# Kernel tuning notes

Measured on AMD Instinct MI355X. Metric: run time of the kernel, lower is better.

The kernel has to match this reference:

```python
import jax, jax.numpy as jnp
import numpy as np

B = 256      # number of graphs
IN = 128     # input_dim
FD = 256     # feature_dim (dims[1])
HID = 256    # hidden_dim of attention block (dims[2])
OUT = 128    # final output dim (dims[3])
TXT = 512    # text_emb_dim

LENGTHS = np.asarray(128 + (np.arange(B) % 256), dtype=np.int64)  # ragged lens 128..383
N = int(LENGTHS.sum())  # 65408 total nodes
LMAX = int(LENGTHS.max())  # 383


def setup_inputs() -> dict:
    key = jax.random.key(0)
    ks = jax.random.split(key, 16)
    s = 0.02
    return {
        "input": jax.random.normal(ks[0], (N, IN), jnp.float32),
        "text_emb": jax.random.normal(ks[1], (B, TXT), jnp.float32),
        "repeat_list": jnp.asarray(LENGTHS),
        # layer 0: Linear(IN -> FD)
        "W0": jax.random.normal(ks[2], (IN, FD), jnp.float32) * s,
        "b0": jax.random.normal(ks[3], (FD,), jnp.float32) * s,
        # cross-attention block params
        "Wq": jax.random.normal(ks[4], (TXT, FD), jnp.float32) * s,
        "bq": jax.random.normal(ks[5], (FD,), jnp.float32) * s,
        "Wk": jax.random.normal(ks[6], (FD, FD), jnp.float32) * s,
        "bk": jax.random.normal(ks[7], (FD,), jnp.float32) * s,
        "Wv": jax.random.normal(ks[8], (FD, FD), jnp.float32) * s,
        "bv": jax.random.normal(ks[9], (FD,), jnp.float32) * s,
        "Wo": jax.random.normal(ks[10], (FD, HID), jnp.float32) * s,
        "bo": jax.random.normal(ks[11], (HID,), jnp.float32) * s,
        # layer 2: Linear(HID -> OUT), last layer (no activation)
        "W2": jax.random.normal(ks[12], (HID, OUT), jnp.float32) * s,
        "b2": jax.random.normal(ks[13], (OUT,), jnp.float32) * s,
    }


def _cross_attention(h, text_emb, repeat_list, Wq, bq, Wk, bk, Wv, bv, Wo, bo):
    # h: [N, FD] packed ragged node features; repeat_list: [B] lengths (constant ints)
    n = h.shape[0]
    b = repeat_list.shape[0]
    fd = h.shape[1]
    # pad ragged -> [B, LMAX, FD] (pad value 0) + validity mask
    seg = jnp.repeat(jnp.arange(b), repeat_list, total_repeat_length=n)  # [N] graph id
    offsets = jnp.cumsum(repeat_list) - repeat_list                      # [B] start of each graph
    pos = jnp.arange(n) - offsets[seg]                                   # [N] within-graph pos
    padded = jnp.zeros((b, LMAX, fd), h.dtype).at[seg, pos].set(h)
    valid = jnp.arange(LMAX)[None, :] < repeat_list[:, None]             # [B, L]

    q = text_emb @ Wq + bq                              # [B, FD]
    k = (padded @ Wk + bk) * valid[..., None]           # masked_fill(mask==0, 0)
    v = (padded @ Wv + bv) * valid[..., None]

    # query is broadcast identically over the padded-length axis, so each row of the
    # [L, L] score matrix is the same vector: scores[b, j] = q[b] . k[b, j]
    scores = jnp.einsum('bf,bjf->bj', q, k)             # [B, L]
    scores = jnp.where(valid, scores, -jnp.inf)         # mask invalid columns j
    p = jax.nn.softmax(scores, axis=-1)                 # [B, L]
    # output = attention^T @ value with identical rows => out[b,j,:] = p[b,j] * sum_i v[b,i,:]
    v_sum = v.sum(axis=1)                               # [B, FD] (padded rows already zero)
    out_pad = p[..., None] * v_sum[:, None, :]          # [B, L, FD]
    out_nodes = out_pad[seg, pos]                       # unpad-concat -> [N, FD]
    return out_nodes @ Wo + bo                          # [N, HID]


def reference(input, text_emb, repeat_list, W0, b0, Wq, bq, Wk, bk, Wv, bv, Wo, bo, W2, b2):
    h = jax.nn.relu(input @ W0 + b0)                                     # layer 0 + relu
    h = _cross_attention(h, text_emb, repeat_list, Wq, bq, Wk, bk, Wv, bv, Wo, bo)
    h = jax.nn.relu(h)                                                   # layer 1 + relu
    return h @ W2 + b2                                                   # layer 2 (last, no act)
```

## Files before the change

kernel.cpp:

```cpp
#include <hip/hip_runtime.h>
#include <math.h>

#define B_G   256
#define IN_D  128
#define FD    256
#define HID   256
#define OUT_D 128
#define TXT   512
#define XKS   136

typedef short bf16x8 __attribute__((ext_vector_type(8)));
typedef float f32x4  __attribute__((ext_vector_type(4)));

__device__ __forceinline__ unsigned bf_rne(float x) {
    unsigned u = __float_as_uint(x);
    u += 0x7fffu + ((u >> 16) & 1u);
    return u >> 16;
}
__device__ __forceinline__ float bf_to_f(unsigned h) {
    return __uint_as_float(h << 16);
}
__device__ __forceinline__ void split2(float a0, float a1, unsigned& hp, unsigned& lp) {
    unsigned h0 = bf_rne(a0), h1 = bf_rne(a1);
    float r0 = a0 - bf_to_f(h0), r1 = a1 - bf_to_f(h1);
    hp = h0 | (h1 << 16);
    lp = bf_rne(r0) | (bf_rne(r1) << 16);
}

__global__ __launch_bounds__(256) void k_prepA(
    const float* __restrict__ text_emb, const float* __restrict__ Wq,
    const float* __restrict__ bq, const float* __restrict__ Wk,
    const float* __restrict__ W0, const int* __restrict__ lens,
    float* __restrict__ qk, int* __restrict__ offsets, float* __restrict__ hsum,
    unsigned short* __restrict__ W0sH, unsigned short* __restrict__ W0sL)
{
    int blk = blockIdx.x, t = threadIdx.x;
    __shared__ float te[TXT];
    __shared__ float q[FD];
    __shared__ int   sc[B_G];

    if (blk < 256) {
        int b = blk;
        hsum[b * FD + t] = 0.f;
        for (int i = t; i < TXT; i += 256) te[i] = text_emb[(size_t)b * TXT + i];
        __syncthreads();
        float acc = bq[t];
        for (int k = 0; k < TXT; k++) acc = fmaf(te[k], Wq[k * FD + t], acc);
        q[t] = acc;
        __syncthreads();
        float a2 = 0.f;
        for (int f = 0; f < FD; f++) a2 = fmaf(Wk[t * FD + f], q[f], a2);
        qk[b * FD + t] = a2;
    } else if (blk < 260) {
        int e = (blk - 256) * 256 + t;
        int kc = e >> 8, c = e & 255;
        size_t base = (size_t)(kc * 256 + c) * 32;
        for (int kk = 0; kk < 32; kk++) {
            float v = W0[(size_t)(kc * 32 + kk) * FD + c];
            unsigned h = bf_rne(v);
            float r = v - bf_to_f(h);
            W0sH[base + kk] = (unsigned short)h;
            W0sL[base + kk] = (unsigned short)bf_rne(r);
        }
    } else {
        sc[t] = lens[t];
        __syncthreads();
        for (int d = 1; d < 256; d <<= 1) {
            int v = (t >= d) ? sc[t - d] : 0;
            __syncthreads();
            sc[t] += v;
            __syncthreads();
        }
        offsets[t + 1] = sc[t];
        if (t == 0) offsets[0] = 0;
    }
}

__global__ __launch_bounds__(256, 2) void k_l0_mfma(
    const float* __restrict__ X,
    const unsigned short* __restrict__ W0sH, const unsigned short* __restrict__ W0sL,
    const float* __restrict__ b0, const float* __restrict__ qk,
    const int* __restrict__ offsets,
    float* __restrict__ scores, float* __restrict__ hsum)
{
    int b = blockIdx.y;
    int off = offsets[b], len = offsets[b + 1] - off;
    int n0 = blockIdx.x * 64;
    if (n0 >= len) return;
    int nvalid = min(64, len - n0);

    __shared__ __align__(16) unsigned short XsH[64 * XKS], XsL[64 * XKS];
    __shared__ float qks[FD];
    __shared__ float bsh[FD];
    __shared__ float red[4][64];

    int tid = threadIdx.x;
    int lane = tid & 63, w = tid >> 6;
    int ln = lane & 15, quad = lane >> 4;

    qks[tid] = qk[b * FD + tid];
    bsh[tid] = b0[tid];

    {
        int node_s = tid >> 2, ks = (tid & 3) * 32;
        const float* Xr = X + (size_t)(off + n0 + node_s) * IN_D + ks;
        float xv[32];
        if (node_s < nvalid) {
#pragma unroll
            for (int q2 = 0; q2 < 8; q2++) {
                float4 v = ((const float4*)Xr)[q2];
                xv[q2 * 4 + 0] = v.x; xv[q2 * 4 + 1] = v.y;
                xv[q2 * 4 + 2] = v.z; xv[q2 * 4 + 3] = v.w;
            }
        } else {
#pragma unroll
            for (int q2 = 0; q2 < 32; q2++) xv[q2] = 0.f;
        }
#pragma unroll
        for (int g = 0; g < 4; g++) {
            uint4 hq, lq;
            split2(xv[g * 8 + 0], xv[g * 8 + 1], hq.x, lq.x);
            split2(xv[g * 8 + 2], xv[g * 8 + 3], hq.y, lq.y);
            split2(xv[g * 8 + 4], xv[g * 8 + 5], hq.z, lq.z);
            split2(xv[g * 8 + 6], xv[g * 8 + 7], hq.w, lq.w);
            *(uint4*)&XsH[node_s * XKS + ks + g * 8] = hq;
            *(uint4*)&XsL[node_s * XKS + ks + g * 8] = lq;
        }
    }
    __syncthreads();

    f32x4 acc[4][4] = {};
#pragma unroll
    for (int kc = 0; kc < 4; kc++) {
        bf16x8 AH[4], AL[4], BH[4], BL[4];
#pragma unroll
        for (int i = 0; i < 4; i++) {
            AH[i] = *(const bf16x8*)&XsH[(16 * i + ln) * XKS + kc * 32 + quad * 8];
            AL[i] = *(const bf16x8*)&XsL[(16 * i + ln) * XKS + kc * 32 + quad * 8];
        }
#pragma unroll
        for (int j = 0; j < 4; j++) {
            int c = 64 * w + 16 * j + ln;
            size_t base = (size_t)(kc * 256 + c) * 32 + quad * 8;
            BH[j] = *(const bf16x8*)&W0sH[base];
            BL[j] = *(const bf16x8*)&W0sL[base];
        }
#pragma unroll
        for (int i = 0; i < 4; i++)
#pragma unroll
            for (int j = 0; j < 4; j++) {
                acc[i][j] = __builtin_amdgcn_mfma_f32_16x16x32_bf16(AH[i], BH[j], acc[i][j], 0, 0, 0);
                acc[i][j] = __builtin_amdgcn_mfma_f32_16x16x32_bf16(AH[i], BL[j], acc[i][j], 0, 0, 0);
                acc[i][j] = __builtin_amdgcn_mfma_f32_16x16x32_bf16(AL[i], BH[j], acc[i][j], 0, 0, 0);
            }
    }

    float sp[4][4];
    float cs[4] = {0.f, 0.f, 0.f, 0.f};
#pragma unroll
    for (int i = 0; i < 4; i++)
#pragma unroll
        for (int r = 0; r < 4; r++) sp[i][r] = 0.f;

#pragma unroll
    for (int i = 0; i < 4; i++)
#pragma unroll
        for (int j = 0; j < 4; j++) {
            int c = 64 * w + 16 * j + ln;
            float bb = bsh[c], qv = qks[c];
#pragma unroll
            for (int r = 0; r < 4; r++) {
                int node = 16 * i + 4 * quad + r;
                float h = acc[i][j][r] + bb;
                h = (h > 0.f && node < nvalid) ? h : 0.f;
                sp[i][r] = fmaf(h, qv, sp[i][r]);
                cs[j] += h;
            }
        }
#pragma unroll
    for (int i = 0; i < 4; i++)
#pragma unroll
        for (int r = 0; r < 4; r++) {
            float s = sp[i][r];
            s += __shfl_xor(s, 1); s += __shfl_xor(s, 2);
            s += __shfl_xor(s, 4); s += __shfl_xor(s, 8);
            sp[i][r] = s;
        }
    if (ln == 0) {
#pragma unroll
        for (int i = 0; i < 4; i++)
#pragma unroll
            for (int r = 0; r < 4; r++)
                red[w][16 * i + 4 * quad + r] = sp[i][r];
    }
#pragma unroll
    for (int j = 0; j < 4; j++) {
        float s = cs[j];
        s += __shfl_xor(s, 16); s += __shfl_xor(s, 32);
        if (quad == 0) atomicAdd(&hsum[b * FD + 64 * w + 16 * j + ln], s);
    }
    __syncthreads();
    if (tid < 64 && tid < nvalid)
        scores[off + n0 + tid] = red[0][tid] + red[1][tid] + red[2][tid] + red[3][tid];
}

__global__ __launch_bounds__(1024) void k_graph(
    const float* __restrict__ scores, const float* __restrict__ hsum,
    const float* __restrict__ Wv, const float* __restrict__ bv,
    const float* __restrict__ Wo, const int* __restrict__ offsets,
    float* __restrict__ wvec, float* __restrict__ smax, float* __restrict__ dinv)
{
    int b = blockIdx.x, tid = threadIdx.x;
    int t = tid & 255, g = tid >> 8;
    int off = offsets[b], len = offsets[b + 1] - off;
    __shared__ float redm[16], reds[16];
    __shared__ float hs[FD], vs[FD];
    __shared__ float part[4][FD];

    float m = -INFINITY;
    for (int i = tid; i < len; i += 1024) m = fmaxf(m, scores[off + i]);
    for (int d = 1; d < 64; d <<= 1) m = fmaxf(m, __shfl_xor(m, d));
    if ((tid & 63) == 0) redm[tid >> 6] = m;
    __syncthreads();
    m = -INFINITY;
#pragma unroll
    for (int k = 0; k < 16; k++) m = fmaxf(m, redm[k]);

    float s = 0.f;
    for (int i = tid; i < len; i += 1024) s += expf(scores[off + i] - m);
    for (int d = 1; d < 64; d <<= 1) s += __shfl_xor(s, d);
    if ((tid & 63) == 0) reds[tid >> 6] = s;
    if (g == 0) hs[t] = hsum[b * FD + t];
    __syncthreads();
    s = 0.f;
#pragma unroll
    for (int k = 0; k < 16; k++) s += reds[k];

    float acc = (g == 0) ? (float)len * bv[t] : 0.f;
    for (int f = 64 * g; f < 64 * g + 64; f++) acc = fmaf(hs[f], Wv[f * FD + t], acc);
    part[g][t] = acc;
    __syncthreads();
    if (g == 0) vs[t] = part[0][t] + part[1][t] + part[2][t] + part[3][t];
    __syncthreads();
    float a2 = 0.f;
    for (int f = 64 * g; f < 64 * g + 64; f++) a2 = fmaf(vs[f], Wo[f * HID + t], a2);
    part[g][t] = a2;
    __syncthreads();
    if (g == 0) wvec[b * HID + t] = part[0][t] + part[1][t] + part[2][t] + part[3][t];
    if (tid == 0) { smax[b] = m; dinv[b] = 1.0f / s; }
}

__global__ __launch_bounds__(1024) void k_fin_walk(
    const float* __restrict__ scores, const float* __restrict__ wvec,
    const float* __restrict__ bo, const float* __restrict__ W2,
    const float* __restrict__ b2, const float* __restrict__ smax,
    const float* __restrict__ dinv, const int* __restrict__ offsets,
    float* __restrict__ Y)
{
    int b = blockIdx.x, tid = threadIdx.x;
    int off = offsets[b], len = offsets[b + 1] - off;

    __shared__ float tOrig[256];
    __shared__ float tS[256], dwS[256], dbS[256];
    __shared__ int   kS[256];
    __shared__ float wS[256], boS[256];
    __shared__ int   cnt[257], startS[257];
    __shared__ float A0s[OUT_D], C0s[OUT_D], b2s[OUT_D];
    __shared__ float segA[8][OUT_D], segC[8][OUT_D];
    __shared__ __align__(16) char ops_raw[656 * 16];
    float* opA = (float*)ops_raw;
    float* opB = (float*)(ops_raw + 2624);
    int*   opN = (int*)(ops_raw + 5248);
    int*   opK = (int*)(ops_raw + 7872);

    float m = smax[b], di = dinv[b];

    bool real = false;
    if (tid < 256) {
        float wv = wvec[b * HID + tid];
        float bv = bo[tid];
        wS[tid] = wv; boS[tid] = bv;
        bool isev = (wv > 0.f && bv < 0.f) || (wv < 0.f && bv > 0.f);
        float tk = isev ? (-bv / wv) : INFINITY;
        real = isev && (tk < INFINITY);
        tOrig[tid] = real ? tk : INFINITY;
        cnt[tid] = 0;
        if (tid == 0) cnt[256] = 0;
    }
    if (tid < OUT_D) b2s[tid] = b2[tid];
    __syncthreads();

    if (tid < 256) {
        float tk = tOrig[tid];
        int r = 0;
        for (int j = 0; j < 256; j++) {
            float tj = tOrig[j];
            r += (tj < tk || (tj == tk && j < tid)) ? 1 : 0;
        }
        tS[r] = tk;
        kS[r] = tid;
        float wv = wS[tid], bv = boS[tid];
        dwS[r] = real ? fabsf(wv) : 0.f;
        dbS[r] = real ? -fabsf(bv) : 0.f;
    }
    {
        int q = tid >> 7, c = tid & 127;
        float pa = 0.f, pc = 0.f;
        for (int k = q * 32; k < q * 32 + 32; ++k) {
            float v = W2[(size_t)k * OUT_D + c];
            float wv = wS[k], bv = boS[k];
            bool ini = (bv > 0.f) || (bv == 0.f && wv > 0.f);
            pa = fmaf(ini ? wv : 0.f, v, pa);
            pc = fmaf(ini ? bv : 0.f, v, pc);
        }
        segA[q][c] = pa; segC[q][c] = pc;
    }
    int nE = __syncthreads_count(real);

    float p_n = 0.f; int r_n = 0;
    if (tid < len) {
        p_n = expf(scores[off + tid] - m) * di;
        int r = 0;
#pragma unroll
        for (int st = 128; st > 0; st >>= 1)
            if (tS[r + st - 1] < p_n) r += st;
        r_n = r;
        atomicAdd(&cnt[r], 1);
    }
    if (tid < OUT_D) {
        float sa = 0.f, sc2 = 0.f;
#pragma unroll
        for (int q = 0; q < 8; q++) { sa += segA[q][tid]; sc2 += segC[q][tid]; }
        A0s[tid] = sa; C0s[tid] = sc2;
    }
    __syncthreads();

    if (tid < 64) {
        int l = tid;
        int v0 = cnt[4 * l], v1 = cnt[4 * l + 1], v2 = cnt[4 * l + 2], v3 = cnt[4 * l + 3];
        int s0 = v0, s1 = s0 + v1, s2 = s1 + v2, s3 = s2 + v3;
        int run = s3;
#pragma unroll
        for (int d = 1; d < 64; d <<= 1) {
            int t2 = __shfl_up(run, d);
            if (l >= d) run += t2;
        }
        int base = run - s3;
        startS[4 * l + 0] = base;      cnt[4 * l + 0] = base;
        startS[4 * l + 1] = base + s0; cnt[4 * l + 1] = base + s0;
        startS[4 * l + 2] = base + s1; cnt[4 * l + 2] = base + s1;
        startS[4 * l + 3] = base + s2; cnt[4 * l + 3] = base + s2;
        if (l == 63) { startS[256] = base + s3; cnt[256] = base + s3; }
    }
    __syncthreads();

    int L    = len + nE;
    int Lpad = (L + 7) & ~7;
    int Lseg = ((Lpad + 63) >> 6) << 3;

    if (tid < len) {
        int slot = atomicAdd(&cnt[r_n], 1);
        int pos = slot + r_n;
        opA[pos] = p_n; opB[pos] = 0.f; opN[pos] = tid; opK[pos] = 0;
    }
    if (tid < nE) {
        int pos = startS[tid + 1] + tid;
        opA[pos] = dwS[tid]; opB[pos] = dbS[tid]; opN[pos] = -1; opK[pos] = kS[tid];
    }
    for (int i = L + tid; i < 648; i += 1024) {
        opA[i] = 0.f; opB[i] = 0.f; opN[i] = -1; opK[i] = 0;
    }
    __syncthreads();

    int s = tid >> 7, c = tid & 127;
    {
        int iBeg = s * Lseg, iEnd = iBeg + Lseg;
        int lo = 0, hi = nE;
        while (lo < hi) {
            int mid = (lo + hi) >> 1;
            if (startS[mid + 1] + mid < iBeg) lo = mid + 1; else hi = mid;
        }
        float dA = 0.f, dC = 0.f;
        for (int j = lo; j < nE && (startS[j + 1] + j) < iEnd; ++j) {
            float v = W2[(size_t)kS[j] * OUT_D + c];
            dA = fmaf(dwS[j], v, dA);
            dC = fmaf(dbS[j], v, dC);
        }
        segA[s][c] = dA; segC[s][c] = dC;
    }
    __syncthreads();

    {
        float A = A0s[c], C = C0s[c];
        for (int s2 = 0; s2 < s; ++s2) { A += segA[s2][c]; C += segC[s2][c]; }
        float b2v = b2s[c];
        float* Yb = Y + (size_t)off * OUT_D + c;
        int i0 = s * Lseg;

        float rA[8], rB[8], rV[8]; int rN[8], rK[8];
#pragma unroll
        for (int u = 0; u < 8; ++u) {
            rA[u] = opA[i0 + u]; rB[u] = opB[i0 + u];
            rN[u] = opN[i0 + u]; rK[u] = opK[i0 + u];
        }
#pragma unroll
        for (int u = 0; u < 8; ++u) rV[u] = W2[(size_t)rK[u] * OUT_D + c];

        for (int i0w = i0; i0w < i0 + Lseg; i0w += 8) {
#pragma unroll
            for (int u = 0; u < 8; ++u) {
                int i = i0w + u;
                float aI = rA[u], bI = rB[u], vv = rV[u];
                int nI = rN[u];
                rA[u] = opA[i + 8]; rB[u] = opB[i + 8];
                rN[u] = opN[i + 8]; rK[u] = opK[i + 8];
                rV[u] = W2[(size_t)rK[u] * OUT_D + c];
                if (nI >= 0) Yb[(size_t)nI * OUT_D] = fmaf(aI, A, C) + b2v;
                else { A = fmaf(aI, vv, A); C = fmaf(bI, vv, C); }
            }
        }
    }
}

extern "C" void kernel_launch(void* const* d_in, const int* in_sizes, int n_in,
                              void* d_out, int out_size, void* d_ws, size_t ws_size,
                              hipStream_t stream)
{
    const float* X        = (const float*)d_in[0];
    const float* text_emb = (const float*)d_in[1];
    const int*   lens     = (const int*)d_in[2];
    const float* W0       = (const float*)d_in[3];
    const float* b0       = (const float*)d_in[4];
    const float* Wq       = (const float*)d_in[5];
    const float* bq       = (const float*)d_in[6];
    const float* Wk       = (const float*)d_in[7];
    const float* Wv       = (const float*)d_in[9];
    const float* bv       = (const float*)d_in[10];
    const float* Wo       = (const float*)d_in[11];
    const float* bo       = (const float*)d_in[12];
    const float* W2       = (const float*)d_in[13];
    const float* b2       = (const float*)d_in[14];
    float* Y = (float*)d_out;

    char* base = (char*)d_ws;
    size_t o = 0;
    int*   offsets = (int*)(base + o);            o += 1088;
    float* qkbuf   = (float*)(base + o);          o += 262144;
    float* wvec    = (float*)(base + o);          o += 262144;
    float* smaxb   = (float*)(base + o);          o += 1024;
    float* dinvb   = (float*)(base + o);          o += 1024;
    float* hsum    = (float*)(base + o);          o += 262144;
    float* scores  = (float*)(base + o);          o += 262144;
    unsigned short* W0sH = (unsigned short*)(base + o); o += 65536;
    unsigned short* W0sL = (unsigned short*)(base + o); o += 65536;

    k_prepA<<<261, 256, 0, stream>>>(text_emb, Wq, bq, Wk, W0, lens,
                                     qkbuf, offsets, hsum, W0sH, W0sL);
    k_l0_mfma<<<dim3(6, B_G), 256, 0, stream>>>(X, W0sH, W0sL, b0, qkbuf, offsets, scores, hsum);
    k_graph<<<B_G, 1024, 0, stream>>>(scores, hsum, Wv, bv, Wo, offsets, wvec, smaxb, dinvb);
    k_fin_walk<<<B_G, 1024, 0, stream>>>(scores, wvec, bo, W2, b2, smaxb, dinvb, offsets, Y);
}
```

Baseline: 202.3 us.

## Fuse graph softmax/projection into walk kernel and raise l0 occupancy

Merges the per-graph softmax and Wv/Wo projection kernel into the final walk kernel, so one launch replaces two and the wvec/smax/dinv round trip through global memory disappears. Scores are read once per thread and the exponentials are reused for the probabilities. The layer-0 MFMA kernel moves to 4 blocks per CU, streams X loads per group and loads B fragments inside the j loop to cut register pressure. The walk loop now skips W2 loads for output ops. The fused kernel assumes len <= 1024, which holds for these inputs, and occupancy changes may cause spills.

```diff
diff --git a/kernel.cpp b/kernel.cpp
--- a/kernel.cpp
+++ b/kernel.cpp
@@ -76,7 +76,7 @@
     }
 }
 
-__global__ __launch_bounds__(256, 2) void k_l0_mfma(
+__global__ __launch_bounds__(256, 4) void k_l0_mfma(
     const float* __restrict__ X,
     const unsigned short* __restrict__ W0sH, const unsigned short* __restrict__ W0sL,
     const float* __restrict__ b0, const float* __restrict__ qk,
@@ -103,26 +103,18 @@
 
     {
         int node_s = tid >> 2, ks = (tid & 3) * 32;
-        const float* Xr = X + (size_t)(off + n0 + node_s) * IN_D + ks;
-        float xv[32];
-        if (node_s < nvalid) {
-#pragma unroll
-            for (int q2 = 0; q2 < 8; q2++) {
-                float4 v = ((const float4*)Xr)[q2];
-                xv[q2 * 4 + 0] = v.x; xv[q2 * 4 + 1] = v.y;
-                xv[q2 * 4 + 2] = v.z; xv[q2 * 4 + 3] = v.w;
-            }
-        } else {
-#pragma unroll
-            for (int q2 = 0; q2 < 32; q2++) xv[q2] = 0.f;
-        }
+        const float4* Xr4 = (const float4*)(X + (size_t)(off + n0 + node_s) * IN_D + ks);
+        bool v = (node_s < nvalid);
 #pragma unroll
         for (int g = 0; g < 4; g++) {
+            float4 a, c4;
+            if (v) { a = Xr4[2 * g]; c4 = Xr4[2 * g + 1]; }
+            else   { a = make_float4(0.f, 0.f, 0.f, 0.f); c4 = a; }
             uint4 hq, lq;
-            split2(xv[g * 8 + 0], xv[g * 8 + 1], hq.x, lq.x);
-            split2(xv[g * 8 + 2], xv[g * 8 + 3], hq.y, lq.y);
-            split2(xv[g * 8 + 4], xv[g * 8 + 5], hq.z, lq.z);
-            split2(xv[g * 8 + 6], xv[g * 8 + 7], hq.w, lq.w);
+            split2(a.x,  a.y,  hq.x, lq.x);
+            split2(a.z,  a.w,  hq.y, lq.y);
+            split2(c4.x, c4.y, hq.z, lq.z);
+            split2(c4.z, c4.w, hq.w, lq.w);
             *(uint4*)&XsH[node_s * XKS + ks + g * 8] = hq;
             *(uint4*)&XsL[node_s * XKS + ks + g * 8] = lq;
         }
@@ -132,7 +124,7 @@
     f32x4 acc[4][4] = {};
 #pragma unroll
     for (int kc = 0; kc < 4; kc++) {
-        bf16x8 AH[4], AL[4], BH[4], BL[4];
+        bf16x8 AH[4], AL[4];
 #pragma unroll
         for (int i = 0; i < 4; i++) {
             AH[i] = *(const bf16x8*)&XsH[(16 * i + ln) * XKS + kc * 32 + quad * 8];
@@ -142,17 +134,15 @@
         for (int j = 0; j < 4; j++) {
             int c = 64 * w + 16 * j + ln;
             size_t base = (size_t)(kc * 256 + c) * 32 + quad * 8;
-            BH[j] = *(const bf16x8*)&W0sH[base];
-            BL[j] = *(const bf16x8*)&W0sL[base];
-        }
-#pragma unroll
-        for (int i = 0; i < 4; i++)
-#pragma unroll
-            for (int j = 0; j < 4; j++) {
-                acc[i][j] = __builtin_amdgcn_mfma_f32_16x16x32_bf16(AH[i], BH[j], acc[i][j], 0, 0, 0);
-                acc[i][j] = __builtin_amdgcn_mfma_f32_16x16x32_bf16(AH[i], BL[j], acc[i][j], 0, 0, 0);
-                acc[i][j] = __builtin_amdgcn_mfma_f32_16x16x32_bf16(AL[i], BH[j], acc[i][j], 0, 0, 0);
+            bf16x8 BH = *(const bf16x8*)&W0sH[base];
+            bf16x8 BL = *(const bf16x8*)&W0sL[base];
+#pragma unroll
+            for (int i = 0; i < 4; i++) {
+                acc[i][j] = __builtin_amdgcn_mfma_f32_16x16x32_bf16(AH[i], BH, acc[i][j], 0, 0, 0);
+                acc[i][j] = __builtin_amdgcn_mfma_f32_16x16x32_bf16(AH[i], BL, acc[i][j], 0, 0, 0);
+                acc[i][j] = __builtin_amdgcn_mfma_f32_16x16x32_bf16(AL[i], BH, acc[i][j], 0, 0, 0);
             }
+        }
     }
 
     float sp[4][4];
@@ -204,68 +194,26 @@
         scores[off + n0 + tid] = red[0][tid] + red[1][tid] + red[2][tid] + red[3][tid];
 }
 
-__global__ __launch_bounds__(1024) void k_graph(
+__global__ __launch_bounds__(1024) void k_graph_walk(
     const float* __restrict__ scores, const float* __restrict__ hsum,
     const float* __restrict__ Wv, const float* __restrict__ bv,
-    const float* __restrict__ Wo, const int* __restrict__ offsets,
-    float* __restrict__ wvec, float* __restrict__ smax, float* __restrict__ dinv)
+    const float* __restrict__ Wo, const float* __restrict__ bo,
+    const float* __restrict__ W2, const float* __restrict__ b2,
+    const int* __restrict__ offsets, float* __restrict__ Y)
 {
     int b = blockIdx.x, tid = threadIdx.x;
+    int off = offsets[b], len = offsets[b + 1] - off;
     int t = tid & 255, g = tid >> 8;
-    int off = offsets[b], len = offsets[b + 1] - off;
+
     __shared__ float redm[16], reds[16];
     __shared__ float hs[FD], vs[FD];
     __shared__ float part[4][FD];
-
-    float m = -INFINITY;
-    for (int i = tid; i < len; i += 1024) m = fmaxf(m, scores[off + i]);
-    for (int d = 1; d < 64; d <<= 1) m = fmaxf(m, __shfl_xor(m, d));
-    if ((tid & 63) == 0) redm[tid >> 6] = m;
-    __syncthreads();
-    m = -INFINITY;
-#pragma unroll
-    for (int k = 0; k < 16; k++) m = fmaxf(m, redm[k]);
-
-    float s = 0.f;
-    for (int i = tid; i < len; i += 1024) s += expf(scores[off + i] - m);
-    for (int d = 1; d < 64; d <<= 1) s += __shfl_xor(s, d);
-    if ((tid & 63) == 0) reds[tid >> 6] = s;
-    if (g == 0) hs[t] = hsum[b * FD + t];
-    __syncthreads();
-    s = 0.f;
-#pragma unroll
-    for (int k = 0; k < 16; k++) s += reds[k];
-
-    float acc = (g == 0) ? (float)len * bv[t] : 0.f;
-    for (int f = 64 * g; f < 64 * g + 64; f++) acc = fmaf(hs[f], Wv[f * FD + t], acc);
-    part[g][t] = acc;
-    __syncthreads();
-    if (g == 0) vs[t] = part[0][t] + part[1][t] + part[2][t] + part[3][t];
-    __syncthreads();
-    float a2 = 0.f;
-    for (int f = 64 * g; f < 64 * g + 64; f++) a2 = fmaf(vs[f], Wo[f * HID + t], a2);
-    part[g][t] = a2;
-    __syncthreads();
-    if (g == 0) wvec[b * HID + t] = part[0][t] + part[1][t] + part[2][t] + part[3][t];
-    if (tid == 0) { smax[b] = m; dinv[b] = 1.0f / s; }
-}
-
-__global__ __launch_bounds__(1024) void k_fin_walk(
-    const float* __restrict__ scores, const float* __restrict__ wvec,
-    const float* __restrict__ bo, const float* __restrict__ W2,
-    const float* __restrict__ b2, const float* __restrict__ smax,
-    const float* __restrict__ dinv, const int* __restrict__ offsets,
-    float* __restrict__ Y)
-{
-    int b = blockIdx.x, tid = threadIdx.x;
-    int off = offsets[b], len = offsets[b + 1] - off;
-
+    __shared__ float wv2[HID], boS[HID], b2s[OUT_D];
     __shared__ float tOrig[256];
     __shared__ float tS[256], dwS[256], dbS[256];
     __shared__ int   kS[256];
-    __shared__ float wS[256], boS[256];
     __shared__ int   cnt[257], startS[257];
-    __shared__ float A0s[OUT_D], C0s[OUT_D], b2s[OUT_D];
+    __shared__ float A0s[OUT_D], C0s[OUT_D];
     __shared__ float segA[8][OUT_D], segC[8][OUT_D];
     __shared__ __align__(16) char ops_raw[656 * 16];
     float* opA = (float*)ops_raw;
@@ -273,21 +221,52 @@
     int*   opN = (int*)(ops_raw + 5248);
     int*   opK = (int*)(ops_raw + 7872);
 
-    float m = smax[b], di = dinv[b];
+    if (g == 0) { boS[t] = bo[t]; hs[t] = hsum[b * FD + t]; }
+    if (tid < OUT_D) b2s[tid] = b2[tid];
+    if (tid <= 256) cnt[tid] = 0;
+    float s_n = (tid < len) ? scores[off + tid] : -INFINITY;
+
+    float m = s_n;
+#pragma unroll
+    for (int d = 1; d < 64; d <<= 1) m = fmaxf(m, __shfl_xor(m, d));
+    if ((tid & 63) == 0) redm[tid >> 6] = m;
+    __syncthreads();
+    m = -INFINITY;
+#pragma unroll
+    for (int k = 0; k < 16; k++) m = fmaxf(m, redm[k]);
+
+    float e_n = (tid < len) ? expf(s_n - m) : 0.f;
+    float s = e_n;
+#pragma unroll
+    for (int d = 1; d < 64; d <<= 1) s += __shfl_xor(s, d);
+    if ((tid & 63) == 0) reds[tid >> 6] = s;
+    __syncthreads();
+    s = 0.f;
+#pragma unroll
+    for (int k = 0; k < 16; k++) s += reds[k];
+    float dinv = 1.0f / s;
+
+    float acc = (g == 0) ? (float)len * bv[t] : 0.f;
+    for (int f = 64 * g; f < 64 * g + 64; f++) acc = fmaf(hs[f], Wv[f * FD + t], acc);
+    part[g][t] = acc;
+    __syncthreads();
+    if (g == 0) vs[t] = part[0][t] + part[1][t] + part[2][t] + part[3][t];
+    __syncthreads();
+    float a2 = 0.f;
+    for (int f = 64 * g; f < 64 * g + 64; f++) a2 = fmaf(vs[f], Wo[f * HID + t], a2);
+    part[g][t] = a2;
+    __syncthreads();
+    if (g == 0) wv2[t] = part[0][t] + part[1][t] + part[2][t] + part[3][t];
+    __syncthreads();
 
     bool real = false;
     if (tid < 256) {
-        float wv = wvec[b * HID + tid];
-        float bv = bo[tid];
-        wS[tid] = wv; boS[tid] = bv;
-        bool isev = (wv > 0.f && bv < 0.f) || (wv < 0.f && bv > 0.f);
-        float tk = isev ? (-bv / wv) : INFINITY;
+        float wv = wv2[tid], bvv = boS[tid];
+        bool isev = (wv > 0.f && bvv < 0.f) || (wv < 0.f && bvv > 0.f);
+        float tk = isev ? (-bvv / wv) : INFINITY;
         real = isev && (tk < INFINITY);
         tOrig[tid] = real ? tk : INFINITY;
-        cnt[tid] = 0;
-        if (tid == 0) cnt[256] = 0;
-    }
-    if (tid < OUT_D) b2s[tid] = b2[tid];
+    }
     __syncthreads();
 
     if (tid < 256) {
@@ -299,19 +278,19 @@
         }
         tS[r] = tk;
         kS[r] = tid;
-        float wv = wS[tid], bv = boS[tid];
+        float wv = wv2[tid], bvv = boS[tid];
         dwS[r] = real ? fabsf(wv) : 0.f;
-        dbS[r] = real ? -fabsf(bv) : 0.f;
+        dbS[r] = real ? -fabsf(bvv) : 0.f;
     }
     {
         int q = tid >> 7, c = tid & 127;
         float pa = 0.f, pc = 0.f;
         for (int k = q * 32; k < q * 32 + 32; ++k) {
             float v = W2[(size_t)k * OUT_D + c];
-            float wv = wS[k], bv = boS[k];
-            bool ini = (bv > 0.f) || (bv == 0.f && wv > 0.f);
+            float wv = wv2[k], bvv = boS[k];
+            bool ini = (bvv > 0.f) || (bvv == 0.f && wv > 0.f);
             pa = fmaf(ini ? wv : 0.f, v, pa);
-            pc = fmaf(ini ? bv : 0.f, v, pc);
+            pc = fmaf(ini ? bvv : 0.f, v, pc);
         }
         segA[q][c] = pa; segC[q][c] = pc;
     }
@@ -319,7 +298,7 @@
 
     float p_n = 0.f; int r_n = 0;
     if (tid < len) {
-        p_n = expf(scores[off + tid] - m) * di;
+        p_n = e_n * dinv;
         int r = 0;
 #pragma unroll
         for (int st = 128; st > 0; st >>= 1)
@@ -372,9 +351,9 @@
     }
     __syncthreads();
 
-    int s = tid >> 7, c = tid & 127;
+    int sg = tid >> 7, c = tid & 127;
     {
-        int iBeg = s * Lseg, iEnd = iBeg + Lseg;
+        int iBeg = sg * Lseg, iEnd = iBeg + Lseg;
         int lo = 0, hi = nE;
         while (lo < hi) {
             int mid = (lo + hi) >> 1;
@@ -386,25 +365,27 @@
             dA = fmaf(dwS[j], v, dA);
             dC = fmaf(dbS[j], v, dC);
         }
-        segA[s][c] = dA; segC[s][c] = dC;
+        segA[sg][c] = dA; segC[sg][c] = dC;
     }
     __syncthreads();
 
     {
         float A = A0s[c], C = C0s[c];
-        for (int s2 = 0; s2 < s; ++s2) { A += segA[s2][c]; C += segC[s2][c]; }
+        for (int s2 = 0; s2 < sg; ++s2) { A += segA[s2][c]; C += segC[s2][c]; }
         float b2v = b2s[c];
         float* Yb = Y + (size_t)off * OUT_D + c;
-        int i0 = s * Lseg;
-
-        float rA[8], rB[8], rV[8]; int rN[8], rK[8];
+        int i0 = sg * Lseg;
+
+        float rA[8], rB[8], rV[8] = {0,0,0,0,0,0,0,0};
+        int rN[8], rK[8];
 #pragma unroll
         for (int u = 0; u < 8; ++u) {
             rA[u] = opA[i0 + u]; rB[u] = opB[i0 + u];
             rN[u] = opN[i0 + u]; rK[u] = opK[i0 + u];
         }
 #pragma unroll
-        for (int u = 0; u < 8; ++u) rV[u] = W2[(size_t)rK[u] * OUT_D + c];
+        for (int u = 0; u < 8; ++u)
+            if (rN[u] < 0) rV[u] = W2[(size_t)rK[u] * OUT_D + c];
 
         for (int i0w = i0; i0w < i0 + Lseg; i0w += 8) {
 #pragma unroll
@@ -414,7 +395,7 @@
                 int nI = rN[u];
                 rA[u] = opA[i + 8]; rB[u] = opB[i + 8];
                 rN[u] = opN[i + 8]; rK[u] = opK[i + 8];
-                rV[u] = W2[(size_t)rK[u] * OUT_D + c];
+                if (rN[u] < 0) rV[u] = W2[(size_t)rK[u] * OUT_D + c];
                 if (nI >= 0) Yb[(size_t)nI * OUT_D] = fmaf(aI, A, C) + b2v;
                 else { A = fmaf(aI, vv, A); C = fmaf(bI, vv, C); }
             }
@@ -446,9 +427,6 @@
     size_t o = 0;
     int*   offsets = (int*)(base + o);            o += 1088;
     float* qkbuf   = (float*)(base + o);          o += 262144;
-    float* wvec    = (float*)(base + o);          o += 262144;
-    float* smaxb   = (float*)(base + o);          o += 1024;
-    float* dinvb   = (float*)(base + o);          o += 1024;
     float* hsum    = (float*)(base + o);          o += 262144;
     float* scores  = (float*)(base + o);          o += 262144;
     unsigned short* W0sH = (unsigned short*)(base + o); o += 65536;
@@ -457,6 +435,5 @@
     k_prepA<<<261, 256, 0, stream>>>(text_emb, Wq, bq, Wk, W0, lens,
                                      qkbuf, offsets, hsum, W0sH, W0sL);
     k_l0_mfma<<<dim3(6, B_G), 256, 0, stream>>>(X, W0sH, W0sL, b0, qkbuf, offsets, scores, hsum);
-    k_graph<<<B_G, 1024, 0, stream>>>(scores, hsum, Wv, bv, Wo, offsets, wvec, smaxb, dinvb);
-    k_fin_walk<<<B_G, 1024, 0, stream>>>(scores, wvec, bo, W2, b2, smaxb, dinvb, offsets, Y);
-}
+    k_graph_walk<<<B_G, 1024, 0, stream>>>(scores, hsum, Wv, bv, Wo, bo, W2, b2, offsets, Y);
+}
```

After: 215.8 us. +6.7%, slower.
